# Performance work log

Measured on AMD Instinct MI355X. Metric: run time of the kernel, lower is better.

The kernel has to match this reference:

```python
import jax, jax.numpy as jnp
import numpy as np

STACK_DEPTH = 16
SHARPEN = 5.0
LN_EPS = 1e-5
EPS = 1e-8


def _apply_tools(x, tw):
    # tools: relu, gelu(exact), tanh, sigmoid, identity; tw: [B, 5]
    return (jax.nn.relu(x) * tw[:, 0:1]
            + jax.nn.gelu(x, approximate=False) * tw[:, 1:2]
            + jnp.tanh(x) * tw[:, 2:3]
            + jax.nn.sigmoid(x) * tw[:, 3:4]
            + x * tw[:, 4:5])


def _forward(hidden_states, W_proj, b_proj, W_op, b_op, W_tool, b_tool, ln_gamma, ln_beta):
    B, S, H = hidden_states.shape
    D = STACK_DEPTH

    # Per-timestep linear ops are time-independent -> batch them up front.
    proj = jnp.einsum('bsh,ph->bsp', hidden_states, W_proj) + b_proj  # [B,S,2H]
    h_all, v_all = proj[..., :H], proj[..., H:]
    op_probs = jax.nn.softmax(jnp.einsum('bsh,oh->bso', hidden_states, W_op) + b_op, axis=-1)  # [B,S,3]
    tool_w = jax.nn.softmax(jnp.einsum('bsh,th->bst', h_all, W_tool) + b_tool, axis=-1)  # [B,S,T]

    # Differentiable stack recurrence (push/pop/nop with pointer sharpening).
    stack0 = jnp.zeros((B, D, H), hidden_states.dtype)
    pointer0 = jnp.zeros((B, D), hidden_states.dtype).at[:, 0].set(1.0)

    def step(carry, xs):
        stack, pointer = carry
        value, ops = xs  # value: [B,H], ops: [B,3]
        push, pop, nop = ops[:, 0:1], ops[:, 1:2], ops[:, 2:3]
        p_push = jnp.roll(pointer, 1, axis=1)   # pointer moves up on push
        p_pop = jnp.roll(pointer, -1, axis=1)   # pointer moves down on pop
        new_p = push * p_push + pop * p_pop + nop * pointer
        new_p = new_p ** SHARPEN
        new_p = new_p / (jnp.sum(new_p, axis=1, keepdims=True) + EPS)
        w = (push * p_push)[..., None]          # [B,D,1] write weight at pushed slot
        new_stack = stack * (1.0 - w) + value[:, None, :] * w
        top = jnp.sum(new_stack * new_p[..., None], axis=1)  # [B,H]
        return (new_stack, new_p), top

    (stack_f, pointer_f), tops = jax.lax.scan(
        step, (stack0, pointer0),
        (jnp.swapaxes(v_all, 0, 1), jnp.swapaxes(op_probs, 0, 1)))
    tops = jnp.swapaxes(tops, 0, 1)  # [B,S,H]

    processed = jax.vmap(_apply_tools, in_axes=(1, 1), out_axes=1)(tops, tool_w)  # [B,S,H]
    combined = h_all + processed + hidden_states

    mu = jnp.mean(combined, axis=-1, keepdims=True)
    var = jnp.mean((combined - mu) ** 2, axis=-1, keepdims=True)
    final = (combined - mu) * jax.lax.rsqrt(var + LN_EPS) * ln_gamma + ln_beta
    return final, stack_f, pointer_f, tool_w


def setup_inputs() -> dict:
    key = jax.random.key(0)
    ks = jax.random.split(key, 4)
    B, S, H, T = 16, 2048, 1024, 5
    sd = 1.0 / np.sqrt(H)
    return {
        'hidden_states': jax.random.normal(ks[0], (B, S, H), jnp.float32),
        'W_proj': jax.random.normal(ks[1], (2 * H, H), jnp.float32) * sd,
        'b_proj': jnp.zeros((2 * H,), jnp.float32),
        'W_op': jax.random.normal(ks[2], (3, H), jnp.float32) * sd,
        'b_op': jnp.zeros((3,), jnp.float32),
        'W_tool': jax.random.normal(ks[3], (T, H), jnp.float32) * sd,
        'b_tool': jnp.zeros((T,), jnp.float32),
        'ln_gamma': jnp.ones((H,), jnp.float32),
        'ln_beta': jnp.zeros((H,), jnp.float32),
    }


def reference(hidden_states, W_proj, b_proj, W_op, b_op, W_tool, b_tool, ln_gamma, ln_beta):
    return _forward(hidden_states, W_proj, b_proj, W_op, b_op, W_tool, b_tool, ln_gamma, ln_beta)
```

## Files before the change

kernel.cpp:

```cpp
#include <hip/hip_runtime.h>
#include <hip/hip_bf16.h>
#include <cstdint>
#include <cstdio>
#include <type_traits>


typedef float f32x4 __attribute__((ext_vector_type(4)));
typedef __bf16 bf8v __attribute__((ext_vector_type(8)));

#define WS_ABF   0ULL
#define WS_WBF   67108864ULL
#define WS_PROJ  71303168ULL
#define WS_OP4   205520896ULL
#define WS_WP    206045184ULL
#define WS_NEED  210239488ULL

#define OUT_FINAL 0
#define OUT_STACK 33554432ULL
#define OUT_PTR   33816576ULL
#define OUT_TOOLW 33816832ULL
#define SLE_OFF    0ULL
#define SSTART_OFF 9437184ULL
#define COEF_OFF   18874368ULL
#define ATOT_OFF   30000000ULL

__device__ __forceinline__ float bf2f(unsigned short u) {
    union { unsigned int i; float f; } v; v.i = ((unsigned int)u) << 16; return v.f;
}
__device__ __forceinline__ unsigned short f2bf(float f) {
    __hip_bfloat16 h = __float2bfloat16(f);
    return __builtin_bit_cast(unsigned short, h);
}
template<int C>
__device__ __forceinline__ float fdpp(float x) {
    return __int_as_float(__builtin_amdgcn_mov_dpp(__float_as_int(x), C, 0xF, 0xF, true));
}
__device__ __forceinline__ void gload_lds16(const void* g, void* l) {
    __builtin_amdgcn_global_load_lds(
        (__attribute__((address_space(1))) void*)(uintptr_t)g,
        (__attribute__((address_space(3))) void*)l,
        16, 0, 0);
}

__global__ __launch_bounds__(256) void k0(const float* __restrict__ hid,
                                          const float* __restrict__ Wp,
                                          const float* __restrict__ Wop,
                                          const float* __restrict__ bop,
                                          unsigned short* __restrict__ Abf,
                                          unsigned short* __restrict__ Wbf,
                                          float4* __restrict__ op4)
{
    const int bid = blockIdx.x, tid = threadIdx.x;
    if (bid < 8192) {
        const int wid = tid >> 6, lane = tid & 63;
        const int row = bid * 4 + wid;
        const float* hrow = hid + (size_t)row * 1024 + lane * 16;
        float xs[16];
        #pragma unroll
        for (int j = 0; j < 4; ++j) {
            float4 t = *(const float4*)(hrow + j * 4);
            xs[j*4+0] = t.x; xs[j*4+1] = t.y; xs[j*4+2] = t.z; xs[j*4+3] = t.w;
        }
        unsigned short us[16];
        #pragma unroll
        for (int j = 0; j < 16; ++j) us[j] = f2bf(xs[j]);
        uint4 ulo, uhi;
        ulo.x = (unsigned)us[0]  | ((unsigned)us[1]  << 16);
        ulo.y = (unsigned)us[2]  | ((unsigned)us[3]  << 16);
        ulo.z = (unsigned)us[4]  | ((unsigned)us[5]  << 16);
        ulo.w = (unsigned)us[6]  | ((unsigned)us[7]  << 16);
        uhi.x = (unsigned)us[8]  | ((unsigned)us[9]  << 16);
        uhi.y = (unsigned)us[10] | ((unsigned)us[11] << 16);
        uhi.z = (unsigned)us[12] | ((unsigned)us[13] << 16);
        uhi.w = (unsigned)us[14] | ((unsigned)us[15] << 16);
        unsigned short* arow = Abf + (size_t)row * 1024 + lane * 16;
        *(uint4*)(arow)     = ulo;
        *(uint4*)(arow + 8) = uhi;
        float pt[3] = {0.f, 0.f, 0.f};
        #pragma unroll
        for (int o = 0; o < 3; ++o) {
            const float* wrow = Wop + o * 1024 + lane * 16;
            #pragma unroll
            for (int j = 0; j < 4; ++j) {
                float4 t = *(const float4*)(wrow + j * 4);
                pt[o] += xs[j*4+0]*t.x + xs[j*4+1]*t.y + xs[j*4+2]*t.z + xs[j*4+3]*t.w;
            }
        }
        #pragma unroll
        for (int o = 0; o < 3; ++o)
            #pragma unroll
            for (int m = 32; m >= 1; m >>= 1) pt[o] += __shfl_xor(pt[o], m);
        if (lane == 0) {
            float l0 = pt[0] + bop[0], l1 = pt[1] + bop[1], l2 = pt[2] + bop[2];
            float mx = fmaxf(l0, fmaxf(l1, l2));
            float e0 = expf(l0 - mx), e1 = expf(l1 - mx), e2 = expf(l2 - mx);
            float inv = 1.0f / (e0 + e1 + e2);
            float4 r; r.x = e0 * inv; r.y = e1 * inv; r.z = e2 * inv; r.w = 0.f;
            op4[row] = r;
        }
    } else {
        const int b2 = bid - 8192;
        const size_t base = (size_t)b2 * 2048 + tid * 8;
        float4 a = *(const float4*)(Wp + base);
        float4 b = *(const float4*)(Wp + base + 4);
        unsigned short vs[8] = { f2bf(a.x), f2bf(a.y), f2bf(a.z), f2bf(a.w),
                                 f2bf(b.x), f2bf(b.y), f2bf(b.z), f2bf(b.w) };
        uint4 u;
        u.x = (unsigned)vs[0] | ((unsigned)vs[1] << 16);
        u.y = (unsigned)vs[2] | ((unsigned)vs[3] << 16);
        u.z = (unsigned)vs[4] | ((unsigned)vs[5] << 16);
        u.w = (unsigned)vs[6] | ((unsigned)vs[7] << 16);
        *(uint4*)(Wbf + base) = u;
    }
}

__global__ __launch_bounds__(512, 2) void k1(const unsigned short* __restrict__ Abf,
                                             const unsigned short* __restrict__ Wbf,
                                             const float* __restrict__ bproj,
                                             unsigned short* __restrict__ proj,
                                             const float4* __restrict__ op4,
                                             float* __restrict__ wpbuf,
                                             float* __restrict__ out)
{
    __shared__ uint4 sm[8192];
    const int bid = blockIdx.x, tid = threadIdx.x;

    if (bid < 4) {
        const int bbase = bid * 4;
        #pragma unroll
        for (int i = 0; i < 16; ++i)
            sm[tid + i * 512] = ((const uint4*)op4)[(size_t)bbase * 2048 + tid + i * 512];
        __syncthreads();
        if (tid >= 64) return;
        __builtin_amdgcn_s_setprio(1);
        const int lane = tid, d = lane & 15, b4 = lane >> 4;
        const int b = bbase + b4;
        const float4* smf = (const float4*)sm + (size_t)b4 * 2048;
        float* wpb  = wpbuf + (size_t)b * 65536;
        float* cob  = out + COEF_OFF + (size_t)b * 32768;
        float* atot = out + ATOT_OFF + (size_t)b * 512;
        const float probe = (float)d;
        const bool ror1_is_push = (fdpp<0x121>(probe) == (float)((d + 15) & 15));
        float p = (d == 0) ? 1.0f : 0.0f;
        float Apre = 1.0f;

        auto run = [&](auto pushc, auto popc) {
            constexpr int PU = decltype(pushc)::value;
            constexpr int PO = decltype(popc)::value;
            float4 o0 = smf[0], o1 = smf[1];
            #pragma unroll 4
            for (int s = 0; s < 2048; ++s) {
                float4 o2 = smf[(s + 2 < 2048) ? (s + 2) : 2047];
                const float push = o0.x, pop = o0.y, nop = o0.z;
                const float ppush = fdpp<PU>(p);
                const float ppop  = fdpp<PO>(p);
                const float w = push * ppush;
                float lin = push * ppush + pop * ppop + nop * p;
                float x2 = lin * lin;
                float x5 = x2 * x2 * lin;
                float sum = x5;
                sum += fdpp<0x128>(sum);
                sum += fdpp<0x124>(sum);
                sum += fdpp<0x122>(sum);
                sum += fdpp<0x121>(sum);
                float pn = x5 * __builtin_amdgcn_rcpf(sum + 1e-8f);
                const float om = 1.0f - w;
                Apre = ((s & 63) == 0) ? om : Apre * om;
                float2 wp; wp.x = w; wp.y = pn;
                *(float2*)(wpb + ((size_t)s * 16 + d) * 2) = wp;
                cob[(size_t)s * 16 + d] = pn * Apre;
                if ((s & 63) == 63) atot[(s >> 6) * 16 + d] = Apre;
                p = pn;
                o0 = o1; o1 = o2;
            }
        };
        if (ror1_is_push)
            run(std::integral_constant<int,0x121>{}, std::integral_constant<int,0x12F>{});
        else
            run(std::integral_constant<int,0x12F>{}, std::integral_constant<int,0x121>{});
        out[OUT_PTR + (size_t)b * 16 + d] = p;
        return;
    }

    const int li = bid - 4;
    const int xcd = li & 7, j = li >> 3;
    const int gm = xcd * 16 + (j >> 3);
    const int gn = j & 7;
    const int wid = tid >> 6, lane = tid & 63;
    const int wm = wid >> 2, wn = wid & 3;
    const size_t row0 = (size_t)gm * 256;
    const size_t col0 = (size_t)gn * 256;
    char* smc = (char*)sm;
    const char* Ab = (const char*)Abf;
    const char* Bb = (const char*)Wbf;
    const int laneR = lane & 15;
    const int laneK = (lane >> 4) * 16;

    f32x4 acc[8][4];
    const f32x4 z = {0.f, 0.f, 0.f, 0.f};
    #pragma unroll
    for (int i = 0; i < 8; ++i)
        #pragma unroll
        for (int jj = 0; jj < 4; ++jj) acc[i][jj] = z;

    auto STAGE = [&](int kt, int slot) {
        #pragma unroll
        for (int hf = 0; hf < 4; ++hf) {
            #pragma unroll
            for (int i = 0; i < 2; ++i) {
                const int idx  = i * 512 + tid;
                const int off  = idx * 16;
                const int soff = off ^ (((off >> 7) & 7) << 4);
                const int irow = soff >> 7;
                const int colb = soff & 127;
                const char* src = (hf < 2)
                    ? (Ab + (row0 + (size_t)(hf * 128 + irow)) * 2048 + (size_t)kt * 128 + colb)
                    : (Bb + (col0 + (size_t)((hf - 2) * 128 + irow)) * 2048 + (size_t)kt * 128 + colb);
                gload_lds16(src, smc + slot * 65536 + hf * 16384 + (i * 512 + wid * 64) * 16);
            }
        }
    };

    STAGE(0, 0);
    int cur = 0;
    #pragma unroll 1
    for (int kt = 0; kt < 16; ++kt) {
        if (kt < 15) {
            STAGE(kt + 1, cur ^ 1);
            asm volatile("s_waitcnt vmcnt(8)" ::: "memory");
        } else {
            asm volatile("s_waitcnt vmcnt(0)" ::: "memory");
        }
        __builtin_amdgcn_sched_barrier(0);
        __builtin_amdgcn_s_barrier();
        const char* Abase = smc + cur * 65536 + wm * 16384;
        const char* Bbase = smc + cur * 65536 + 32768 + (wn >> 1) * 16384;
        const int bro = (wn & 1) * 64;

        bf8v af[4][2], bfr[4][2];
        #pragma unroll
        for (int m2 = 0; m2 < 4; ++m2)
            #pragma unroll
            for (int kk = 0; kk < 2; ++kk) {
                int byt = (m2 * 16 + laneR) * 128 + kk * 64 + laneK;
                byt ^= ((byt >> 7) & 7) << 4;
                af[m2][kk] = *(const bf8v*)(Abase + byt);
            }
        #pragma unroll
        for (int n2 = 0; n2 < 2; ++n2)
            #pragma unroll
            for (int kk = 0; kk < 2; ++kk) {
                int byt = (bro + n2 * 16 + laneR) * 128 + kk * 64 + laneK;
                byt ^= ((byt >> 7) & 7) << 4;
                bfr[n2][kk] = *(const bf8v*)(Bbase + byt);
            }
        __builtin_amdgcn_s_setprio(1);
        #pragma unroll
        for (int m2 = 0; m2 < 4; ++m2)
            #pragma unroll
            for (int n2 = 0; n2 < 2; ++n2)
                #pragma unroll
                for (int kk = 0; kk < 2; ++kk)
                    acc[m2][n2] = __builtin_amdgcn_mfma_f32_16x16x32_bf16(af[m2][kk], bfr[n2][kk], acc[m2][n2], 0, 0, 0);
        __builtin_amdgcn_s_setprio(0);
        __builtin_amdgcn_s_barrier();
        #pragma unroll
        for (int n2 = 2; n2 < 4; ++n2)
            #pragma unroll
            for (int kk = 0; kk < 2; ++kk) {
                int byt = (bro + n2 * 16 + laneR) * 128 + kk * 64 + laneK;
                byt ^= ((byt >> 7) & 7) << 4;
                bfr[n2][kk] = *(const bf8v*)(Bbase + byt);
            }
        __builtin_amdgcn_s_setprio(1);
        #pragma unroll
        for (int m2 = 0; m2 < 4; ++m2)
            #pragma unroll
            for (int n2 = 2; n2 < 4; ++n2)
                #pragma unroll
                for (int kk = 0; kk < 2; ++kk)
                    acc[m2][n2] = __builtin_amdgcn_mfma_f32_16x16x32_bf16(af[m2][kk], bfr[n2][kk], acc[m2][n2], 0, 0, 0);
        __builtin_amdgcn_s_setprio(0);
        __builtin_amdgcn_s_barrier();
        #pragma unroll
        for (int m2 = 0; m2 < 4; ++m2)
            #pragma unroll
            for (int kk = 0; kk < 2; ++kk) {
                int byt = ((64 + m2 * 16 + laneR)) * 128 + kk * 64 + laneK;
                byt ^= ((byt >> 7) & 7) << 4;
                af[m2][kk] = *(const bf8v*)(Abase + byt);
            }
        __builtin_amdgcn_s_setprio(1);
        #pragma unroll
        for (int m2 = 0; m2 < 4; ++m2)
            #pragma unroll
            for (int n2 = 2; n2 < 4; ++n2)
                #pragma unroll
                for (int kk = 0; kk < 2; ++kk)
                    acc[4 + m2][n2] = __builtin_amdgcn_mfma_f32_16x16x32_bf16(af[m2][kk], bfr[n2][kk], acc[4 + m2][n2], 0, 0, 0);
        __builtin_amdgcn_s_setprio(0);
        __builtin_amdgcn_s_barrier();
        __builtin_amdgcn_s_setprio(1);
        #pragma unroll
        for (int m2 = 0; m2 < 4; ++m2)
            #pragma unroll
            for (int n2 = 0; n2 < 2; ++n2)
                #pragma unroll
                for (int kk = 0; kk < 2; ++kk)
                    acc[4 + m2][n2] = __builtin_amdgcn_mfma_f32_16x16x32_bf16(af[m2][kk], bfr[n2][kk], acc[4 + m2][n2], 0, 0, 0);
        __builtin_amdgcn_s_setprio(0);
        __builtin_amdgcn_s_barrier();
        cur ^= 1;
    }
    #pragma unroll
    for (int mr = 0; mr < 8; ++mr) {
        const int rloc = wm * 128 + mr * 16 + ((lane >> 4) * 4);
        #pragma unroll
        for (int nr = 0; nr < 4; ++nr) {
            const size_t col = col0 + wn * 64 + nr * 16 + laneR;
            const float bias = bproj[col];
            #pragma unroll
            for (int jj = 0; jj < 4; ++jj)
                proj[(row0 + rloc + jj) * 2048 + col] = f2bf(acc[mr][nr][jj] + bias);
        }
    }
}

__global__ __launch_bounds__(256) void k2(unsigned short* __restrict__ proj,
                                          const float* __restrict__ wpbuf,
                                          float* __restrict__ sle)
{
    __shared__ unsigned short vlds[2][4096];
    const int bid = blockIdx.x, tid = threadIdx.x;
    const int hg = bid & 3, c = (bid >> 2) & 31, b = bid >> 7;
    const int wid = tid >> 6;
    const char* vbase = (const char*)proj +
        ((size_t)(b * 2048 + c * 64) * 2048 + 1024 + hg * 256) * 2;
    const float* wpb = wpbuf + ((size_t)b * 2048 + c * 64) * 32;
    unsigned short* topb = proj + ((size_t)b * 2048 + c * 64) * 2048 + 1024 + hg * 256 + tid;

    float st[16];
    #pragma unroll
    for (int d = 0; d < 16; ++d) st[d] = 0.f;

    auto STAGE = [&](int sc, int buf) {
        #pragma unroll
        for (int i = 0; i < 2; ++i) {
            const int g = i * 256 + tid;
            gload_lds16(vbase + (size_t)(sc * 16 + (g >> 5)) * 4096 + (g & 31) * 16,
                        (char*)vlds + buf * 8192 + (i * 256 + wid * 64) * 16);
        }
    };
    STAGE(0, 0);
    __syncthreads();
    for (int sc = 0; sc < 4; ++sc) {
        const int cur = sc & 1;
        if (sc < 3) STAGE(sc + 1, cur ^ 1);
        const unsigned short* vl = vlds[cur];
        #pragma unroll 4
        for (int ls = 0; ls < 16; ++ls) {
            const float v = bf2f(vl[ls * 256 + tid]);
            const float4* wp4 = (const float4*)(wpb + (size_t)(sc * 16 + ls) * 32);
            float t0 = 0.f, t1 = 0.f;
            #pragma unroll
            for (int k = 0; k < 8; ++k) {
                float4 q = wp4[k];
                st[2*k]   = fmaf(q.x, v - st[2*k],   st[2*k]);
                st[2*k+1] = fmaf(q.z, v - st[2*k+1], st[2*k+1]);
                t0 = fmaf(q.y, st[2*k],   t0);
                t1 = fmaf(q.w, st[2*k+1], t1);
            }
            topb[(size_t)(sc * 16 + ls) * 2048] = f2bf(t0 + t1);
        }
        __syncthreads();
    }
    float* so = sle + ((size_t)b * 32 + c) * 16 * 1024 + hg * 256 + tid;
    #pragma unroll
    for (int d = 0; d < 16; ++d) so[(size_t)d * 1024] = st[d];
}

__global__ __launch_bounds__(256) void k2b(const float* __restrict__ sle,
                                           const float* __restrict__ atot,
                                           float* __restrict__ sstart)
{
    const int bid = blockIdx.x, tid = threadIdx.x;
    const int hg = bid & 3, d = (bid >> 2) & 15, b = bid >> 6;
    const int h = hg * 256 + tid;
    const float* sb = sle    + ((size_t)b * 512 + d) * 1024 + h;
    float*       so = sstart + ((size_t)b * 512 + d) * 1024 + h;
    const float* ab = atot + (size_t)b * 512 + d;
    float st = 0.f;
    #pragma unroll 4
    for (int c = 0; c < 31; ++c) {
        so[(size_t)c * 16384] = st;
        st = fmaf(ab[c * 16], st, sb[(size_t)c * 16384]);
    }
    so[31ull * 16384] = st;
}

__global__ __launch_bounds__(256) void k3p(unsigned short* __restrict__ proj,
                                           const float* __restrict__ sstart,
                                           const float* __restrict__ coefb,
                                           const float* __restrict__ sle,
                                           const float* __restrict__ atot,
                                           float* __restrict__ out)
{
    __shared__ float ssL[16384];
    __shared__ float cofL[1024];
    const int bid = blockIdx.x, tid = threadIdx.x;
    const int b = bid >> 5, c = bid & 31;
    {
        const float4* ssg = (const float4*)(sstart + (size_t)bid * 16384);
        #pragma unroll
        for (int i = 0; i < 16; ++i)
            ((float4*)ssL)[i * 256 + tid] = ssg[i * 256 + tid];
        ((float4*)cofL)[tid] = ((const float4*)(coefb + (size_t)bid * 1024))[tid];
    }
    __syncthreads();
    const int h0 = tid * 4;
    float ss[16][4];
    #pragma unroll
    for (int d = 0; d < 16; ++d) {
        float4 t = *(const float4*)(ssL + d * 1024 + h0);
        ss[d][0] = t.x; ss[d][1] = t.y; ss[d][2] = t.z; ss[d][3] = t.w;
    }
    unsigned short* trow = proj + ((size_t)(b * 2048 + c * 64)) * 2048 + 1024 + h0;
    #pragma unroll 2
    for (int s = 0; s < 64; ++s) {
        uint2 tu = *(const uint2*)(trow + (size_t)s * 2048);
        float a0 = bf2f(tu.x & 0xffff), a1 = bf2f(tu.x >> 16);
        float a2 = bf2f(tu.y & 0xffff), a3 = bf2f(tu.y >> 16);
        #pragma unroll
        for (int d = 0; d < 16; ++d) {
            const float cf = cofL[s * 16 + d];
            a0 = fmaf(cf, ss[d][0], a0);
            a1 = fmaf(cf, ss[d][1], a1);
            a2 = fmaf(cf, ss[d][2], a2);
            a3 = fmaf(cf, ss[d][3], a3);
        }
        uint2 o;
        o.x = (unsigned)f2bf(a0) | ((unsigned)f2bf(a1) << 16);
        o.y = (unsigned)f2bf(a2) | ((unsigned)f2bf(a3) << 16);
        *(uint2*)(trow + (size_t)s * 2048) = o;
    }
    if (c == 31) {
        #pragma unroll
        for (int d = 0; d < 16; ++d) {
            float4 sl = *(const float4*)(sle + (((size_t)b * 32 + 31) * 16 + d) * 1024 + h0);
            const float A = atot[(size_t)b * 512 + 31 * 16 + d];
            float4 r;
            r.x = fmaf(A, ss[d][0], sl.x); r.y = fmaf(A, ss[d][1], sl.y);
            r.z = fmaf(A, ss[d][2], sl.z); r.w = fmaf(A, ss[d][3], sl.w);
            *(float4*)(out + OUT_STACK + ((size_t)b * 16 + d) * 1024 + h0) = r;
        }
    }
}

__global__ __launch_bounds__(256) void k5(const unsigned short* __restrict__ proj,
                                          const unsigned short* __restrict__ hidbf,
                                          const float* __restrict__ Wtool,
                                          const float* __restrict__ btool,
                                          const float* __restrict__ gamma,
                                          const float* __restrict__ beta,
                                          float* __restrict__ out)
{
    __shared__ float red[4][8];
    const int row = blockIdx.x, tid = threadIdx.x;
    const int wid = tid >> 6, lane = tid & 63;
    const int k0i = tid * 4;
    uint2 hu = *(const uint2*)(proj + (size_t)row * 2048 + k0i);
    float hh[4];
    hh[0] = bf2f(hu.x & 0xffff); hh[1] = bf2f(hu.x >> 16);
    hh[2] = bf2f(hu.y & 0xffff); hh[3] = bf2f(hu.y >> 16);
    uint2 tu = *(const uint2*)(proj + (size_t)row * 2048 + 1024 + k0i);
    float xs[4];
    xs[0] = bf2f(tu.x & 0xffff); xs[1] = bf2f(tu.x >> 16);
    xs[2] = bf2f(tu.y & 0xffff); xs[3] = bf2f(tu.y >> 16);
    uint2 du = *(const uint2*)(hidbf + (size_t)row * 1024 + k0i);
    float hds[4];
    hds[0] = bf2f(du.x & 0xffff); hds[1] = bf2f(du.x >> 16);
    hds[2] = bf2f(du.y & 0xffff); hds[3] = bf2f(du.y >> 16);
    float pt[5];
    #pragma unroll
    for (int t = 0; t < 5; ++t) {
        float4 wv = *(const float4*)(Wtool + t * 1024 + k0i);
        pt[t] = hh[0]*wv.x + hh[1]*wv.y + hh[2]*wv.z + hh[3]*wv.w;
    }
    #pragma unroll
    for (int t = 0; t < 5; ++t)
        #pragma unroll
        for (int m = 32; m >= 1; m >>= 1) pt[t] += __shfl_xor(pt[t], m);
    if (lane == 0) {
        #pragma unroll
        for (int t = 0; t < 5; ++t) red[wid][t] = pt[t];
    }
    __syncthreads();
    float tw[5];
    {
        float lg[5];
        #pragma unroll
        for (int t = 0; t < 5; ++t)
            lg[t] = red[0][t] + red[1][t] + red[2][t] + red[3][t] + btool[t];
        float mx = fmaxf(fmaxf(fmaxf(lg[0], lg[1]), fmaxf(lg[2], lg[3])), lg[4]);
        float se = 0.f;
        #pragma unroll
        for (int t = 0; t < 5; ++t) { tw[t] = expf(lg[t] - mx); se += tw[t]; }
        float inv = 1.0f / se;
        #pragma unroll
        for (int t = 0; t < 5; ++t) tw[t] *= inv;
    }
    if (tid < 5) out[OUT_TOOLW + (size_t)row * 5 + tid] = tw[tid];
    float cj[4];
    #pragma unroll
    for (int j = 0; j < 4; ++j) {
        const float x = xs[j];
        const float rl = fmaxf(x, 0.f);
        const float gl = 0.5f * x * (1.f + erff(x * 0.70710678118654752f));
        const float th = tanhf(x);
        const float sg = 1.f / (1.f + expf(-x));
        const float pr = rl*tw[0] + gl*tw[1] + th*tw[2] + sg*tw[3] + x*tw[4];
        cj[j] = hh[j] + pr + hds[j];
    }
    float s1 = cj[0] + cj[1] + cj[2] + cj[3];
    float s2 = cj[0]*cj[0] + cj[1]*cj[1] + cj[2]*cj[2] + cj[3]*cj[3];
    #pragma unroll
    for (int m = 32; m >= 1; m >>= 1) { s1 += __shfl_xor(s1, m); s2 += __shfl_xor(s2, m); }
    __syncthreads();
    if (lane == 0) { red[wid][0] = s1; red[wid][1] = s2; }
    __syncthreads();
    const float S1 = red[0][0] + red[1][0] + red[2][0] + red[3][0];
    const float S2 = red[0][1] + red[1][1] + red[2][1] + red[3][1];
    const float mu = S1 * (1.f / 1024.f);
    const float var = S2 * (1.f / 1024.f) - mu * mu;
    const float rstd = rsqrtf(var + 1e-5f);
    float4 g4 = *(const float4*)(gamma + k0i);
    float4 b4 = *(const float4*)(beta + k0i);
    float4 res;
    res.x = (cj[0] - mu) * rstd * g4.x + b4.x;
    res.y = (cj[1] - mu) * rstd * g4.y + b4.y;
    res.z = (cj[2] - mu) * rstd * g4.z + b4.z;
    res.w = (cj[3] - mu) * rstd * g4.w + b4.w;
    *(float4*)(out + (size_t)row * 1024 + k0i) = res;
}

extern "C" void kernel_launch(void* const* d_in, const int* in_sizes, int n_in,
                              void* d_out, int out_size, void* d_ws, size_t ws_size,
                              hipStream_t stream)
{
    if (ws_size < WS_NEED) {
        fprintf(stderr, "kernel_launch: ws_size %zu < required %llu\n",
                ws_size, (unsigned long long)WS_NEED);
        return;
    }
    const float* hid = (const float*)d_in[0];
    const float* Wp  = (const float*)d_in[1];
    const float* bp  = (const float*)d_in[2];
    const float* Wop = (const float*)d_in[3];
    const float* bop = (const float*)d_in[4];
    const float* Wtl = (const float*)d_in[5];
    const float* btl = (const float*)d_in[6];
    const float* gam = (const float*)d_in[7];
    const float* bet = (const float*)d_in[8];
    float* out = (float*)d_out;
    char* ws = (char*)d_ws;
    unsigned short* Abf  = (unsigned short*)(ws + WS_ABF);
    unsigned short* Wbf  = (unsigned short*)(ws + WS_WBF);
    unsigned short* proj = (unsigned short*)(ws + WS_PROJ);
    float4* op4 = (float4*)(ws + WS_OP4);
    float* wpbuf = (float*)(ws + WS_WP);
    float* sle    = out + SLE_OFF;
    float* sstart = out + SSTART_OFF;
    float* coefb  = out + COEF_OFF;
    float* atot   = out + ATOT_OFF;

    k0 <<<9216, 256, 0, stream>>>(hid, Wp, Wop, bop, Abf, Wbf, op4);
    k1 <<<1028, 512, 0, stream>>>(Abf, Wbf, bp, proj, op4, wpbuf, out);
    k2 <<<2048, 256, 0, stream>>>(proj, wpbuf, sle);
    k2b<<<1024, 256, 0, stream>>>(sle, atot, sstart);
    k3p<<<512,  256, 0, stream>>>(proj, sstart, coefb, sle, atot, out);
    k5 <<<32768, 256, 0, stream>>>(proj, Abf, Wtl, btl, gam, bet, out);
}
```

Measured before the change: 450.5 us.

## Fold stack-start correction into LayerNorm kernel and split coef computation out of scan

Removes the k3p pass that read the projected values, added the chunk-start stack contribution and wrote them back to bf16. That correction is now applied inside k5 by reading sstart and coef per row, with an XCD-aware row remap so rows of a chunk share cache. The coefficient computation moves from the serial scan blocks into a small parallel kernel k2c, k2b now writes the final stack directly, and sstart/coef move into the workspace. k5 reads the fp32 hidden input instead of the bf16 copy, and the GEMM loads the second A half into separate registers earlier to overlap LDS reads.

New measurement: 565.7 us. 25.6% more time.

```diff
diff --git a/kernel.cpp b/kernel.cpp
--- a/kernel.cpp
+++ b/kernel.cpp
@@ -9,6 +9,8 @@
 typedef __bf16 bf8v __attribute__((ext_vector_type(8)));
 
 #define WS_ABF   0ULL
+#define WS_SST   0ULL
+#define WS_COEF  33554432ULL
 #define WS_WBF   67108864ULL
 #define WS_PROJ  71303168ULL
 #define WS_OP4   205520896ULL
@@ -20,8 +22,6 @@
 #define OUT_PTR   33816576ULL
 #define OUT_TOOLW 33816832ULL
 #define SLE_OFF    0ULL
-#define SSTART_OFF 9437184ULL
-#define COEF_OFF   18874368ULL
 #define ATOT_OFF   30000000ULL
 
 __device__ __forceinline__ float bf2f(unsigned short u) {
@@ -137,7 +137,6 @@
         const int b = bbase + b4;
         const float4* smf = (const float4*)sm + (size_t)b4 * 2048;
         float* wpb  = wpbuf + (size_t)b * 65536;
-        float* cob  = out + COEF_OFF + (size_t)b * 32768;
         float* atot = out + ATOT_OFF + (size_t)b * 512;
         const float probe = (float)d;
         const bool ror1_is_push = (fdpp<0x121>(probe) == (float)((d + 15) & 15));
@@ -168,7 +167,6 @@
                 Apre = ((s & 63) == 0) ? om : Apre * om;
                 float2 wp; wp.x = w; wp.y = pn;
                 *(float2*)(wpb + ((size_t)s * 16 + d) * 2) = wp;
-                cob[(size_t)s * 16 + d] = pn * Apre;
                 if ((s & 63) == 63) atot[(s >> 6) * 16 + d] = Apre;
                 p = pn;
                 o0 = o1; o1 = o2;
@@ -237,7 +235,7 @@
         const char* Bbase = smc + cur * 65536 + 32768 + (wn >> 1) * 16384;
         const int bro = (wn & 1) * 64;
 
-        bf8v af[4][2], bfr[4][2];
+        bf8v af[4][2], afh[4][2], bfr[4][2];
         #pragma unroll
         for (int m2 = 0; m2 < 4; ++m2)
             #pragma unroll
@@ -247,7 +245,7 @@
                 af[m2][kk] = *(const bf8v*)(Abase + byt);
             }
         #pragma unroll
-        for (int n2 = 0; n2 < 2; ++n2)
+        for (int n2 = 0; n2 < 4; ++n2)
             #pragma unroll
             for (int kk = 0; kk < 2; ++kk) {
                 int byt = (bro + n2 * 16 + laneR) * 128 + kk * 64 + laneK;
@@ -265,12 +263,12 @@
         __builtin_amdgcn_s_setprio(0);
         __builtin_amdgcn_s_barrier();
         #pragma unroll
-        for (int n2 = 2; n2 < 4; ++n2)
+        for (int m2 = 0; m2 < 4; ++m2)
             #pragma unroll
             for (int kk = 0; kk < 2; ++kk) {
-                int byt = (bro + n2 * 16 + laneR) * 128 + kk * 64 + laneK;
+                int byt = ((64 + m2 * 16 + laneR)) * 128 + kk * 64 + laneK;
                 byt ^= ((byt >> 7) & 7) << 4;
-                bfr[n2][kk] = *(const bf8v*)(Bbase + byt);
+                afh[m2][kk] = *(const bf8v*)(Abase + byt);
             }
         __builtin_amdgcn_s_setprio(1);
         #pragma unroll
@@ -282,14 +280,6 @@
                     acc[m2][n2] = __builtin_amdgcn_mfma_f32_16x16x32_bf16(af[m2][kk], bfr[n2][kk], acc[m2][n2], 0, 0, 0);
         __builtin_amdgcn_s_setprio(0);
         __builtin_amdgcn_s_barrier();
-        #pragma unroll
-        for (int m2 = 0; m2 < 4; ++m2)
-            #pragma unroll
-            for (int kk = 0; kk < 2; ++kk) {
-                int byt = ((64 + m2 * 16 + laneR)) * 128 + kk * 64 + laneK;
-                byt ^= ((byt >> 7) & 7) << 4;
-                af[m2][kk] = *(const bf8v*)(Abase + byt);
-            }
         __builtin_amdgcn_s_setprio(1);
         #pragma unroll
         for (int m2 = 0; m2 < 4; ++m2)
@@ -297,7 +287,7 @@
             for (int n2 = 2; n2 < 4; ++n2)
                 #pragma unroll
                 for (int kk = 0; kk < 2; ++kk)
-                    acc[4 + m2][n2] = __builtin_amdgcn_mfma_f32_16x16x32_bf16(af[m2][kk], bfr[n2][kk], acc[4 + m2][n2], 0, 0, 0);
+                    acc[4 + m2][n2] = __builtin_amdgcn_mfma_f32_16x16x32_bf16(afh[m2][kk], bfr[n2][kk], acc[4 + m2][n2], 0, 0, 0);
         __builtin_amdgcn_s_setprio(0);
         __builtin_amdgcn_s_barrier();
         __builtin_amdgcn_s_setprio(1);
@@ -307,7 +297,7 @@
             for (int n2 = 0; n2 < 2; ++n2)
                 #pragma unroll
                 for (int kk = 0; kk < 2; ++kk)
-                    acc[4 + m2][n2] = __builtin_amdgcn_mfma_f32_16x16x32_bf16(af[m2][kk], bfr[n2][kk], acc[4 + m2][n2], 0, 0, 0);
+                    acc[4 + m2][n2] = __builtin_amdgcn_mfma_f32_16x16x32_bf16(afh[m2][kk], bfr[n2][kk], acc[4 + m2][n2], 0, 0, 0);
         __builtin_amdgcn_s_setprio(0);
         __builtin_amdgcn_s_barrier();
         cur ^= 1;
@@ -379,9 +369,27 @@
     for (int d = 0; d < 16; ++d) so[(size_t)d * 1024] = st[d];
 }
 
+__global__ __launch_bounds__(64) void k2c(const float* __restrict__ wpbuf,
+                                          float* __restrict__ coefb)
+{
+    const int bid = blockIdx.x, tid = threadIdx.x;
+    if (tid >= 16) return;
+    const int b = bid >> 5, c = bid & 31;
+    const float* wp = wpbuf + (size_t)b * 65536 + (size_t)c * 64 * 32 + tid * 2;
+    float* co = coefb + (size_t)bid * 1024 + tid;
+    float A = 1.f;
+    #pragma unroll 8
+    for (int j = 0; j < 64; ++j) {
+        float2 q = *(const float2*)(wp + j * 32);
+        A *= (1.f - q.x);
+        co[j * 16] = q.y * A;
+    }
+}
+
 __global__ __launch_bounds__(256) void k2b(const float* __restrict__ sle,
                                            const float* __restrict__ atot,
-                                           float* __restrict__ sstart)
+                                           float* __restrict__ sstart,
+                                           float* __restrict__ out)
 {
     const int bid = blockIdx.x, tid = threadIdx.x;
     const int hg = bid & 3, d = (bid >> 2) & 15, b = bid >> 6;
@@ -396,76 +404,27 @@
         st = fmaf(ab[c * 16], st, sb[(size_t)c * 16384]);
     }
     so[31ull * 16384] = st;
-}
-
-__global__ __launch_bounds__(256) void k3p(unsigned short* __restrict__ proj,
-                                           const float* __restrict__ sstart,
-                                           const float* __restrict__ coefb,
-                                           const float* __restrict__ sle,
-                                           const float* __restrict__ atot,
-                                           float* __restrict__ out)
-{
-    __shared__ float ssL[16384];
-    __shared__ float cofL[1024];
-    const int bid = blockIdx.x, tid = threadIdx.x;
-    const int b = bid >> 5, c = bid & 31;
-    {
-        const float4* ssg = (const float4*)(sstart + (size_t)bid * 16384);
-        #pragma unroll
-        for (int i = 0; i < 16; ++i)
-            ((float4*)ssL)[i * 256 + tid] = ssg[i * 256 + tid];
-        ((float4*)cofL)[tid] = ((const float4*)(coefb + (size_t)bid * 1024))[tid];
-    }
-    __syncthreads();
-    const int h0 = tid * 4;
-    float ss[16][4];
-    #pragma unroll
-    for (int d = 0; d < 16; ++d) {
-        float4 t = *(const float4*)(ssL + d * 1024 + h0);
-        ss[d][0] = t.x; ss[d][1] = t.y; ss[d][2] = t.z; ss[d][3] = t.w;
-    }
-    unsigned short* trow = proj + ((size_t)(b * 2048 + c * 64)) * 2048 + 1024 + h0;
-    #pragma unroll 2
-    for (int s = 0; s < 64; ++s) {
-        uint2 tu = *(const uint2*)(trow + (size_t)s * 2048);
-        float a0 = bf2f(tu.x & 0xffff), a1 = bf2f(tu.x >> 16);
-        float a2 = bf2f(tu.y & 0xffff), a3 = bf2f(tu.y >> 16);
-        #pragma unroll
-        for (int d = 0; d < 16; ++d) {
-            const float cf = cofL[s * 16 + d];
-            a0 = fmaf(cf, ss[d][0], a0);
-            a1 = fmaf(cf, ss[d][1], a1);
-            a2 = fmaf(cf, ss[d][2], a2);
-            a3 = fmaf(cf, ss[d][3], a3);
-        }
-        uint2 o;
-        o.x = (unsigned)f2bf(a0) | ((unsigned)f2bf(a1) << 16);
-        o.y = (unsigned)f2bf(a2) | ((unsigned)f2bf(a3) << 16);
-        *(uint2*)(trow + (size_t)s * 2048) = o;
-    }
-    if (c == 31) {
-        #pragma unroll
-        for (int d = 0; d < 16; ++d) {
-            float4 sl = *(const float4*)(sle + (((size_t)b * 32 + 31) * 16 + d) * 1024 + h0);
-            const float A = atot[(size_t)b * 512 + 31 * 16 + d];
-            float4 r;
-            r.x = fmaf(A, ss[d][0], sl.x); r.y = fmaf(A, ss[d][1], sl.y);
-            r.z = fmaf(A, ss[d][2], sl.z); r.w = fmaf(A, ss[d][3], sl.w);
-            *(float4*)(out + OUT_STACK + ((size_t)b * 16 + d) * 1024 + h0) = r;
-        }
-    }
+    const float fin = fmaf(ab[31 * 16], st, sb[31ull * 16384]);
+    out[OUT_STACK + ((size_t)b * 16 + d) * 1024 + h] = fin;
 }
 
 __global__ __launch_bounds__(256) void k5(const unsigned short* __restrict__ proj,
-                                          const unsigned short* __restrict__ hidbf,
+                                          const float* __restrict__ hid,
                                           const float* __restrict__ Wtool,
                                           const float* __restrict__ btool,
                                           const float* __restrict__ gamma,
                                           const float* __restrict__ beta,
+                                          const float* __restrict__ sstart,
+                                          const float* __restrict__ coefb,
                                           float* __restrict__ out)
 {
     __shared__ float red[4][8];
-    const int row = blockIdx.x, tid = threadIdx.x;
+    const int i = blockIdx.x;
+    const int xcd = i & 7, t0 = i >> 3;
+    const int r = t0 & 63, gh = t0 >> 6;
+    const int g = gh * 8 + xcd;
+    const int row = g * 64 + r;
+    const int tid = threadIdx.x;
     const int wid = tid >> 6, lane = tid & 63;
     const int k0i = tid * 4;
     uint2 hu = *(const uint2*)(proj + (size_t)row * 2048 + k0i);
@@ -476,10 +435,21 @@
     float xs[4];
     xs[0] = bf2f(tu.x & 0xffff); xs[1] = bf2f(tu.x >> 16);
     xs[2] = bf2f(tu.y & 0xffff); xs[3] = bf2f(tu.y >> 16);
-    uint2 du = *(const uint2*)(hidbf + (size_t)row * 1024 + k0i);
-    float hds[4];
-    hds[0] = bf2f(du.x & 0xffff); hds[1] = bf2f(du.x >> 16);
-    hds[2] = bf2f(du.y & 0xffff); hds[3] = bf2f(du.y >> 16);
+    {
+        const float* cof = coefb + (size_t)g * 1024 + r * 16;
+        const float* ssb = sstart + (size_t)g * 16384 + k0i;
+        #pragma unroll
+        for (int d = 0; d < 16; ++d) {
+            const float cf = cof[d];
+            float4 sv = *(const float4*)(ssb + (size_t)d * 1024);
+            xs[0] = fmaf(cf, sv.x, xs[0]);
+            xs[1] = fmaf(cf, sv.y, xs[1]);
+            xs[2] = fmaf(cf, sv.z, xs[2]);
+            xs[3] = fmaf(cf, sv.w, xs[3]);
+        }
+    }
+    float4 hd4 = *(const float4*)(hid + (size_t)row * 1024 + k0i);
+    float hds[4] = {hd4.x, hd4.y, hd4.z, hd4.w};
     float pt[5];
     #pragma unroll
     for (int t = 0; t < 5; ++t) {
@@ -567,16 +537,16 @@
     unsigned short* Wbf  = (unsigned short*)(ws + WS_WBF);
     unsigned short* proj = (unsigned short*)(ws + WS_PROJ);
     float4* op4 = (float4*)(ws + WS_OP4);
-    float* wpbuf = (float*)(ws + WS_WP);
+    float* wpbuf  = (float*)(ws + WS_WP);
+    float* sstart = (float*)(ws + WS_SST);
+    float* coefb  = (float*)(ws + WS_COEF);
     float* sle    = out + SLE_OFF;
-    float* sstart = out + SSTART_OFF;
-    float* coefb  = out + COEF_OFF;
     float* atot   = out + ATOT_OFF;
 
     k0 <<<9216, 256, 0, stream>>>(hid, Wp, Wop, bop, Abf, Wbf, op4);
     k1 <<<1028, 512, 0, stream>>>(Abf, Wbf, bp, proj, op4, wpbuf, out);
     k2 <<<2048, 256, 0, stream>>>(proj, wpbuf, sle);
-    k2b<<<1024, 256, 0, stream>>>(sle, atot, sstart);
-    k3p<<<512,  256, 0, stream>>>(proj, sstart, coefb, sle, atot, out);
-    k5 <<<32768, 256, 0, stream>>>(proj, Abf, Wtl, btl, gam, bet, out);
-}
+    k2c<<<512,  64,  0, stream>>>(wpbuf, coefb);
+    k2b<<<1024, 256, 0, stream>>>(sle, atot, sstart, out);
+    k5 <<<32768, 256, 0, stream>>>(proj, hid, Wtl, btl, gam, bet, sstart, coefb, out);
+}
```
